# Optimization experiments

Hardware: AMD Instinct MI355X
Metric: run time of the kernel (lower is better)

The kernel has to match this reference:

```python
import jax, jax.numpy as jnp
import numpy as np

H, DH = 8, 16  # num_heads, head_dim (out_feats // num_heads)
NP, NA, NS = 100000, 60000, 1000


def _gat_conv(feat_src, feat_dst, n_dst, src, dst, W, al, ar, b):
    # DGL GATConv (eval mode: feat_drop/attn_drop are identity)
    hs = (feat_src @ W).reshape(-1, H, DH)          # [Ns,H,D]
    hd = (feat_dst @ W).reshape(-1, H, DH)          # [Nd,H,D]
    el = (hs * al).sum(-1)                          # [Ns,H]
    er = (hd * ar).sum(-1)                          # [Nd,H]
    e = jax.nn.leaky_relu(el[src] + er[dst], negative_slope=0.2)  # [E,H]
    # segment softmax over edges sharing a destination node
    emax = jax.ops.segment_max(e, dst, num_segments=n_dst)
    emax = jnp.where(jnp.isfinite(emax), emax, 0.0)
    ee = jnp.exp(e - emax[dst])
    denom = jax.ops.segment_sum(ee, dst, num_segments=n_dst)
    alpha = ee / jnp.maximum(denom[dst], 1e-9)      # [E,H]
    m = jax.ops.segment_sum(alpha[:, :, None] * hs[src], dst, num_segments=n_dst)
    return m.reshape(n_dst, H * DH) + b             # [Nd, out_feats]


def setup_inputs() -> dict:
    key = jax.random.key(0)
    ks = jax.random.split(key, 18)
    Epa, Eps = 300000, 150000
    f32 = jnp.float32
    inp = {
        "feat_paper_0": jax.random.normal(ks[0], (NP, 128), f32),
        "feat_author_0": jax.random.normal(ks[1], (NA, 128), f32),
        "feat_subject_0": jax.random.normal(ks[2], (NS, 128), f32),
        "feat_paper_1": jax.random.normal(ks[3], (NP, 128), f32),
        "feat_author_1": jax.random.normal(ks[4], (NA, 128), f32),
        "feat_subject_1": jax.random.normal(ks[5], (NS, 128), f32),
        "pa_src": jax.random.randint(ks[6], (Epa,), 0, NP, jnp.int32),
        "pa_dst": jax.random.randint(ks[7], (Epa,), 0, NA, jnp.int32),
        "ap_src": jax.random.randint(ks[8], (Epa,), 0, NA, jnp.int32),
        "ap_dst": jax.random.randint(ks[9], (Epa,), 0, NP, jnp.int32),
        "ps_src": jax.random.randint(ks[10], (Eps,), 0, NP, jnp.int32),
        "ps_dst": jax.random.randint(ks[11], (Eps,), 0, NS, jnp.int32),
        "sp_src": jax.random.randint(ks[12], (Eps,), 0, NS, jnp.int32),
        "sp_dst": jax.random.randint(ks[13], (Eps,), 0, NP, jnp.int32),
        "Ws": jax.random.normal(ks[14], (4, 128, 128), f32) * 0.08,
        "als": jax.random.normal(ks[15], (4, H, DH), f32) * 0.1,
        "ars": jax.random.normal(ks[16], (4, H, DH), f32) * 0.1,
        "bs": jnp.zeros((4, 128), f32),
    }
    return inp


def reference(feat_paper_0, feat_author_0, feat_subject_0,
              feat_paper_1, feat_author_1, feat_subject_1,
              pa_src, pa_dst, ap_src, ap_dst, ps_src, ps_dst, sp_src, sp_dst,
              Ws, als, ars, bs):
    def one_input(fp, fa, fs):
        # rel 0: paper->author, 1: author->paper, 2: paper->subject, 3: subject->paper
        h_author = _gat_conv(fp, fa, NA, pa_src, pa_dst, Ws[0], als[0], ars[0], bs[0])
        h_paper_ap = _gat_conv(fa, fp, NP, ap_src, ap_dst, Ws[1], als[1], ars[1], bs[1])
        h_subject = _gat_conv(fp, fs, NS, ps_src, ps_dst, Ws[2], als[2], ars[2], bs[2])
        h_paper_sp = _gat_conv(fs, fp, NP, sp_src, sp_dst, Ws[3], als[3], ars[3], bs[3])
        h_paper = (h_paper_ap + h_paper_sp) * 0.5  # HeteroGraphConv aggregate='mean'
        # act = identity; key order for ACM: [paper, author, subject]
        return jnp.concatenate([h_paper, h_author, h_subject], axis=0)

    out0 = one_input(feat_paper_0, feat_author_0, feat_subject_0)
    out1 = one_input(feat_paper_1, feat_author_1, feat_subject_1)
    return jnp.stack([out0, out1], axis=0)  # [2, NP+NA+NS, 128]
```

## Files before the change

### kernel.cpp

```cpp
#include <hip/hip_runtime.h>

#define NHEAD 8
#define NPAPER 100000
#define NAUTHOR 60000
#define NSUBJ 1000
#define NTOT (NPAPER + NAUTHOR + NSUBJ)
#define NDEG 261000

typedef __attribute__((ext_vector_type(8))) short bf16x8;
typedef __attribute__((ext_vector_type(4))) float f32x4;
typedef __attribute__((ext_vector_type(4))) unsigned int u32x4;

__device__ __forceinline__ unsigned short f2bf(float x) {
    unsigned int u = __builtin_bit_cast(unsigned int, x);
    u += 0x7fffu + ((u >> 16) & 1u);
    return (unsigned short)(u >> 16);
}
__device__ __forceinline__ float bf2f_lo(unsigned int v) {
    return __builtin_bit_cast(float, v << 16);
}
__device__ __forceinline__ float bf2f_hi(unsigned int v) {
    return __builtin_bit_cast(float, v & 0xffff0000u);
}

__global__ void prep_kernel(const float* __restrict__ Ws, const float* __restrict__ als,
                            const float* __restrict__ ars,
                            unsigned short* __restrict__ Wt,
                            unsigned short* __restrict__ combo, int* __restrict__ deg) {
    int b = blockIdx.x;
    if (b >= 288) {
        int idx = (b - 288) * 1024 + threadIdx.x * 4;
        if (idx < NDEG) *reinterpret_cast<int4*>(&deg[idx]) = int4{0, 0, 0, 0};
        return;
    }
    int idx = b * 256 + threadIdx.x;
    if (idx < 65536) {
        int r = idx >> 14, rem = idx & 16383, c = rem >> 7, k = rem & 127;
        Wt[idx] = f2bf(Ws[(r << 14) + k * 128 + c]);
    } else if (idx < 65536 + 8192) {
        int j = idx - 65536;
        int r = j >> 11, rem = j & 2047, n = rem >> 7, k = rem & 127;
        int p = r ^ 1;
        const float *W, *a;
        if (n < 8) {
            W = Ws + (r << 14) + k * 128 + n * 16;
            a = als + r * 128 + n * 16;
        } else {
            int h = n - 8;
            W = Ws + (p << 14) + k * 128 + h * 16;
            a = ars + p * 128 + h * 16;
        }
        float s = 0.f;
#pragma unroll
        for (int d = 0; d < 16; ++d) s += W[d] * a[d];
        combo[j] = f2bf(s);
    }
}

__device__ __forceinline__ void stage_W(unsigned short* Wl, const unsigned short* Wt,
                                        const unsigned short* cb, int tid) {
#pragma unroll
    for (int it = 0; it < 9; ++it) {
        int id = it * 256 + tid;
        int r = id >> 4, c8 = id & 15;
        const unsigned short* srcp = (r < 128) ? (Wt + r * 128) : (cb + (r - 128) * 128);
        uint4 v = *reinterpret_cast<const uint4*>(srcp + c8 * 8);
        *reinterpret_cast<uint4*>(&Wl[(r * 16 + (c8 ^ (r & 15))) * 8]) = v;
    }
}

__device__ __forceinline__ void mfma_set(const unsigned short* Wl, unsigned short* Abf,
                                         const bf16x8* af, int tid, int row0, int N,
                                         float* __restrict__ el, float* __restrict__ er) {
    const int l = tid & 63, w = tid >> 6, lrow = l & 15, lk8 = l >> 4;
#pragma unroll
    for (int t9 = 0; t9 < 9; ++t9) {
        f32x4 acc = f32x4{0.f, 0.f, 0.f, 0.f};
#pragma unroll
        for (int ks = 0; ks < 4; ++ks) {
            int wrow = t9 * 16 + lrow;
            int c8 = ks * 4 + lk8;
            bf16x8 bf = *reinterpret_cast<const bf16x8*>(
                &Wl[(wrow * 16 + (c8 ^ (wrow & 15))) * 8]);
            acc = __builtin_amdgcn_mfma_f32_16x16x32_bf16(af[ks], bf, acc, 0, 0, 0);
        }
        if (t9 < 8) {
#pragma unroll
            for (int r = 0; r < 4; ++r) {
                int rl = w * 16 + lk8 * 4 + r;
                int col = t9 * 16 + lrow;
                Abf[(rl * 16 + ((col >> 3) ^ (rl & 15))) * 8 + (col & 7)] = f2bf(acc[r]);
            }
        } else {
#pragma unroll
            for (int r = 0; r < 4; ++r) {
                int row = row0 + w * 16 + lk8 * 4 + r;
                if (row < N) {
                    if (lrow < 8) el[(size_t)row * 8 + lrow] = acc[r];
                    else er[(size_t)row * 8 + (lrow - 8)] = acc[r];
                }
            }
        }
    }
}

__device__ __forceinline__ void store_hs(const unsigned short* Abf,
                                         unsigned short* __restrict__ hs, int tid,
                                         int row0, int N) {
#pragma unroll
    for (int it = 0; it < 4; ++it) {
        int id = it * 256 + tid;
        int r = id >> 4, c8 = id & 15;
        int row = row0 + r;
        if (row < N) {
            uint4 v = *reinterpret_cast<const uint4*>(&Abf[(r * 16 + (c8 ^ (r & 15))) * 8]);
            *reinterpret_cast<uint4*>(hs + (size_t)row * 128 + c8 * 8) = v;
        }
    }
}

struct PCArgs {
    const int* edst[4];
    int ebase[5];
    int nbase[4];
    int* deg;
    int cblk;
    const float* A[6];
    int N[6];
    int blk0[7];
    const unsigned short* Wt1[6];
    const unsigned short* cb1[6];
    unsigned short* hs1[6];
    float* el1[6];
    float* er1[6];
    const unsigned short* Wt2[6];
    const unsigned short* cb2[6];
    unsigned short* hs2[6];
    float* el2[6];
    float* er2[6];
    int has2[6];
};

__global__ __launch_bounds__(256) void project_count(PCArgs a) {
    __shared__ unsigned short Abf[64 * 128];
    __shared__ unsigned short Wl[144 * 128];
    int bb = blockIdx.x;
    const int tid = threadIdx.x;
    if (bb < a.cblk) {
        int idx = bb * 256 + tid;
        if (idx < a.ebase[4]) {
            int r = 0;
            while (idx >= a.ebase[r + 1]) ++r;
            atomicAdd(&a.deg[a.nbase[r] + a.edst[r][idx - a.ebase[r]]], 1);
        }
        return;
    }
    bb -= a.cblk;
    int t = 0;
    while (bb >= a.blk0[t + 1]) ++t;
    const int row0 = (bb - a.blk0[t]) * 64;
    const int N = a.N[t];
    const float* A = a.A[t];

#pragma unroll
    for (int it = 0; it < 4; ++it) {
        int id = it * 256 + tid;
        int r = id >> 4, c8 = id & 15;
        int row = row0 + r;
        if (row >= N) row = N - 1;
        const f32x4* ap = reinterpret_cast<const f32x4*>(A + (size_t)row * 128 + c8 * 8);
        f32x4 v0 = __builtin_nontemporal_load(ap);
        f32x4 v1 = __builtin_nontemporal_load(ap + 1);
        uint4 pk;
        pk.x = (unsigned)f2bf(v0.x) | ((unsigned)f2bf(v0.y) << 16);
        pk.y = (unsigned)f2bf(v0.z) | ((unsigned)f2bf(v0.w) << 16);
        pk.z = (unsigned)f2bf(v1.x) | ((unsigned)f2bf(v1.y) << 16);
        pk.w = (unsigned)f2bf(v1.z) | ((unsigned)f2bf(v1.w) << 16);
        *reinterpret_cast<uint4*>(&Abf[(r * 16 + (c8 ^ (r & 15))) * 8]) = pk;
    }
    stage_W(Wl, a.Wt1[t], a.cb1[t], tid);
    __syncthreads();

    const int l = tid & 63, w = tid >> 6, lrow = l & 15, lk8 = l >> 4;
    bf16x8 af[4];
    const int arow = w * 16 + lrow;
#pragma unroll
    for (int ks = 0; ks < 4; ++ks) {
        int c8 = ks * 4 + lk8;
        af[ks] = *reinterpret_cast<const bf16x8*>(
            &Abf[(arow * 16 + (c8 ^ (arow & 15))) * 8]);
    }
    __syncthreads();

    mfma_set(Wl, Abf, af, tid, row0, N, a.el1[t], a.er1[t]);
    __syncthreads();
    store_hs(Abf, a.hs1[t], tid, row0, N);
    if (!a.has2[t]) return;
    stage_W(Wl, a.Wt2[t], a.cb2[t], tid);
    __syncthreads();
    mfma_set(Wl, Abf, af, tid, row0, N, a.el2[t], a.er2[t]);
    __syncthreads();
    store_hs(Abf, a.hs2[t], tid, row0, N);
}

__global__ __launch_bounds__(256) void scan_bsum(const int* __restrict__ deg,
                                                 int* __restrict__ bsums, int N) {
    int base = blockIdx.x * 1024 + threadIdx.x * 4;
    int s = 0;
#pragma unroll
    for (int j = 0; j < 4; ++j) {
        int i = base + j;
        if (i < N) s += deg[i];
    }
#pragma unroll
    for (int off = 32; off; off >>= 1) s += __shfl_down(s, off);
    __shared__ int wt[4];
    if ((threadIdx.x & 63) == 0) wt[threadIdx.x >> 6] = s;
    __syncthreads();
    if (threadIdx.x == 0) bsums[blockIdx.x] = wt[0] + wt[1] + wt[2] + wt[3];
}

__global__ __launch_bounds__(256) void scan_final(const int* __restrict__ deg,
                                                  const int* __restrict__ bsums,
                                                  int* __restrict__ row_ptr,
                                                  int* __restrict__ cursor, int N) {
    int t = threadIdx.x;
    __shared__ int s_start;
    __shared__ int wsum[4];
    {
        int acc = 0;
        for (int i = t; i < (int)blockIdx.x; i += 256) acc += bsums[i];
#pragma unroll
        for (int off = 32; off; off >>= 1) acc += __shfl_down(acc, off);
        if ((t & 63) == 0) wsum[t >> 6] = acc;
        __syncthreads();
        if (t == 0) s_start = wsum[0] + wsum[1] + wsum[2] + wsum[3];
        __syncthreads();
    }
    int base = blockIdx.x * 1024 + t * 4;
    int d[4];
    int s = 0;
#pragma unroll
    for (int j = 0; j < 4; ++j) {
        int i = base + j;
        d[j] = (i < N) ? deg[i] : 0;
        s += d[j];
    }
    int inc = s;
#pragma unroll
    for (int off = 1; off < 64; off <<= 1) {
        int u = __shfl_up(inc, off);
        if ((t & 63) >= off) inc += u;
    }
    __shared__ int wt[4];
    if ((t & 63) == 63) wt[t >> 6] = inc;
    __syncthreads();
    int start = s_start;
    for (int w = 0; w < (t >> 6); ++w) start += wt[w];
    start += inc - s;
#pragma unroll
    for (int j = 0; j < 4; ++j) {
        int i = base + j;
        if (i < N) {
            row_ptr[i] = start;
            cursor[i] = start;
        }
        start += d[j];
    }
    if (base < N && base + 4 >= N) row_ptr[N] = start;
}

struct CsrPtrs {
    const int* esrc[4];
    const int* edst[4];
    int ebase[5];
    int nbase[4];
};

__global__ void csr_scatter(CsrPtrs cp, int* __restrict__ cursor,
                            int* __restrict__ srcs) {
    int idx = blockIdx.x * 256 + threadIdx.x;
    if (idx >= cp.ebase[4]) return;
    int r = 0;
    while (idx >= cp.ebase[r + 1]) ++r;
    int e = idx - cp.ebase[r];
    int p = atomicAdd(&cursor[cp.nbase[r] + cp.edst[r][e]], 1);
    srcs[p] = cp.esrc[r][e];
}

__device__ __forceinline__ void acc_dual(
    int p0, int p1, float erd0, float erd1, int l, int h,
    const int* __restrict__ srcs,
    const float* __restrict__ el0, const float* __restrict__ el1,
    const unsigned short* __restrict__ hs0, const unsigned short* __restrict__ hs1,
    float* A0, float* A1, float& DS0, float& DS1) {
    float a0[8], a1[8];
#pragma unroll
    for (int j = 0; j < 8; ++j) { a0[j] = 0.f; a1[j] = 0.f; }
    float d0 = 0.f, d1 = 0.f;
    int p = p0;
    for (; p + 4 <= p1; p += 4) {
        int sx[4];
#pragma unroll
        for (int u = 0; u < 4; ++u) sx[u] = srcs[p + u];
        float ev0[4], ev1[4];
        uint4 q0[4], q1[4];
#pragma unroll
        for (int u = 0; u < 4; ++u) {
            ev0[u] = el0[(size_t)sx[u] * 8 + h] + erd0;
            ev1[u] = el1[(size_t)sx[u] * 8 + h] + erd1;
            q0[u] = *reinterpret_cast<const uint4*>(hs0 + (size_t)sx[u] * 128 + l * 8);
            q1[u] = *reinterpret_cast<const uint4*>(hs1 + (size_t)sx[u] * 128 + l * 8);
        }
#pragma unroll
        for (int u = 0; u < 4; ++u) {
            float e0 = ev0[u];
            e0 = e0 > 0.f ? e0 : 0.2f * e0;
            float ee0 = __expf(e0);
            d0 += ee0;
            a0[0] += ee0 * bf2f_lo(q0[u].x);
            a0[1] += ee0 * bf2f_hi(q0[u].x);
            a0[2] += ee0 * bf2f_lo(q0[u].y);
            a0[3] += ee0 * bf2f_hi(q0[u].y);
            a0[4] += ee0 * bf2f_lo(q0[u].z);
            a0[5] += ee0 * bf2f_hi(q0[u].z);
            a0[6] += ee0 * bf2f_lo(q0[u].w);
            a0[7] += ee0 * bf2f_hi(q0[u].w);
            float e1 = ev1[u];
            e1 = e1 > 0.f ? e1 : 0.2f * e1;
            float ee1 = __expf(e1);
            d1 += ee1;
            a1[0] += ee1 * bf2f_lo(q1[u].x);
            a1[1] += ee1 * bf2f_hi(q1[u].x);
            a1[2] += ee1 * bf2f_lo(q1[u].y);
            a1[3] += ee1 * bf2f_hi(q1[u].y);
            a1[4] += ee1 * bf2f_lo(q1[u].z);
            a1[5] += ee1 * bf2f_hi(q1[u].z);
            a1[6] += ee1 * bf2f_lo(q1[u].w);
            a1[7] += ee1 * bf2f_hi(q1[u].w);
        }
    }
    for (; p < p1; ++p) {
        int s = srcs[p];
        float e0 = el0[(size_t)s * 8 + h] + erd0;
        float e1 = el1[(size_t)s * 8 + h] + erd1;
        uint4 q0 = *reinterpret_cast<const uint4*>(hs0 + (size_t)s * 128 + l * 8);
        uint4 q1 = *reinterpret_cast<const uint4*>(hs1 + (size_t)s * 128 + l * 8);
        e0 = e0 > 0.f ? e0 : 0.2f * e0;
        float ee0 = __expf(e0);
        d0 += ee0;
        a0[0] += ee0 * bf2f_lo(q0.x);
        a0[1] += ee0 * bf2f_hi(q0.x);
        a0[2] += ee0 * bf2f_lo(q0.y);
        a0[3] += ee0 * bf2f_hi(q0.y);
        a0[4] += ee0 * bf2f_lo(q0.z);
        a0[5] += ee0 * bf2f_hi(q0.z);
        a0[6] += ee0 * bf2f_lo(q0.w);
        a0[7] += ee0 * bf2f_hi(q0.w);
        e1 = e1 > 0.f ? e1 : 0.2f * e1;
        float ee1 = __expf(e1);
        d1 += ee1;
        a1[0] += ee1 * bf2f_lo(q1.x);
        a1[1] += ee1 * bf2f_hi(q1.x);
        a1[2] += ee1 * bf2f_lo(q1.y);
        a1[3] += ee1 * bf2f_hi(q1.y);
        a1[4] += ee1 * bf2f_lo(q1.z);
        a1[5] += ee1 * bf2f_hi(q1.z);
        a1[6] += ee1 * bf2f_lo(q1.w);
        a1[7] += ee1 * bf2f_hi(q1.w);
    }
#pragma unroll
    for (int j = 0; j < 8; ++j) { A0[j] = a0[j]; A1[j] = a1[j]; }
    DS0 = d0;
    DS1 = d1;
}

__device__ __forceinline__ void nt_store2(float* op, f32x4 o0, f32x4 o1) {
    f32x4* vp = reinterpret_cast<f32x4*>(op);
    __builtin_nontemporal_store(o0, vp);
    __builtin_nontemporal_store(o1, vp + 1);
}

#define PB2 6250
#define AB2 3750
#define SB2 1000

struct AggArgs {
    const int* rp;
    const int* srcs;
    const float* el[8];
    const float* er[8];
    const unsigned short* hs[8];
    const float* bs;
    float* out0;
    float* out1;
};

__global__ __launch_bounds__(256) void mega_agg(AggArgs a) {
    int blk = blockIdx.x;
    __shared__ float Am[16][128];
    __shared__ float Dm[16][8];

    if (blk < PB2) {
        int dst = blk * 16 + (threadIdx.x >> 4);
        int l = threadIdx.x & 15, h = l >> 1;
        if (dst >= NPAPER) return;
        float A1_0[8], A1_1[8], d1_0, d1_1;
        acc_dual(a.rp[60000 + dst], a.rp[60000 + dst + 1],
                 a.er[1][(size_t)dst * 8 + h], a.er[5][(size_t)dst * 8 + h], l, h,
                 a.srcs, a.el[1], a.el[5], a.hs[1], a.hs[5], A1_0, A1_1, d1_0, d1_1);
        float A3_0[8], A3_1[8], d3_0, d3_1;
        acc_dual(a.rp[161000 + dst], a.rp[161000 + dst + 1],
                 a.er[3][(size_t)dst * 8 + h], a.er[7][(size_t)dst * 8 + h], l, h,
                 a.srcs, a.el[3], a.el[7], a.hs[3], a.hs[7], A3_0, A3_1, d3_0, d3_1);
        const float4* bp1 = reinterpret_cast<const float4*>(a.bs + 128 + l * 8);
        const float4* bp3 = reinterpret_cast<const float4*>(a.bs + 384 + l * 8);
        float4 b10 = bp1[0], b11 = bp1[1], b30 = bp3[0], b31 = bp3[1];
        float i1 = 1.f / fmaxf(d1_0, 1e-9f);
        float i3 = 1.f / fmaxf(d3_0, 1e-9f);
        f32x4 o0, o1;
        o0.x = 0.5f * ((A1_0[0] * i1 + b10.x) + (A3_0[0] * i3 + b30.x));
        o0.y = 0.5f * ((A1_0[1] * i1 + b10.y) + (A3_0[1] * i3 + b30.y));
        o0.z = 0.5f * ((A1_0[2] * i1 + b10.z) + (A3_0[2] * i3 + b30.z));
        o0.w = 0.5f * ((A1_0[3] * i1 + b10.w) + (A3_0[3] * i3 + b30.w));
        o1.x = 0.5f * ((A1_0[4] * i1 + b11.x) + (A3_0[4] * i3 + b31.x));
        o1.y = 0.5f * ((A1_0[5] * i1 + b11.y) + (A3_0[5] * i3 + b31.y));
        o1.z = 0.5f * ((A1_0[6] * i1 + b11.z) + (A3_0[6] * i3 + b31.z));
        o1.w = 0.5f * ((A1_0[7] * i1 + b11.w) + (A3_0[7] * i3 + b31.w));
        nt_store2(a.out0 + (size_t)dst * 128 + l * 8, o0, o1);
        i1 = 1.f / fmaxf(d1_1, 1e-9f);
        i3 = 1.f / fmaxf(d3_1, 1e-9f);
        o0.x = 0.5f * ((A1_1[0] * i1 + b10.x) + (A3_1[0] * i3 + b30.x));
        o0.y = 0.5f * ((A1_1[1] * i1 + b10.y) + (A3_1[1] * i3 + b30.y));
        o0.z = 0.5f * ((A1_1[2] * i1 + b10.z) + (A3_1[2] * i3 + b30.z));
        o0.w = 0.5f * ((A1_1[3] * i1 + b10.w) + (A3_1[3] * i3 + b30.w));
        o1.x = 0.5f * ((A1_1[4] * i1 + b11.x) + (A3_1[4] * i3 + b31.x));
        o1.y = 0.5f * ((A1_1[5] * i1 + b11.y) + (A3_1[5] * i3 + b31.y));
        o1.z = 0.5f * ((A1_1[6] * i1 + b11.z) + (A3_1[6] * i3 + b31.z));
        o1.w = 0.5f * ((A1_1[7] * i1 + b11.w) + (A3_1[7] * i3 + b31.w));
        nt_store2(a.out1 + (size_t)dst * 128 + l * 8, o0, o1);
    } else if (blk < PB2 + AB2) {
        int dst = (blk - PB2) * 16 + (threadIdx.x >> 4);
        int l = threadIdx.x & 15, h = l >> 1;
        if (dst >= NAUTHOR) return;
        float A0[8], A1[8], d0, d1;
        acc_dual(a.rp[dst], a.rp[dst + 1],
                 a.er[0][(size_t)dst * 8 + h], a.er[4][(size_t)dst * 8 + h], l, h,
                 a.srcs, a.el[0], a.el[4], a.hs[0], a.hs[4], A0, A1, d0, d1);
        const float4* bp = reinterpret_cast<const float4*>(a.bs + l * 8);
        float4 b0 = bp[0], b1 = bp[1];
        float inv = 1.f / fmaxf(d0, 1e-9f);
        f32x4 o0 = {A0[0] * inv + b0.x, A0[1] * inv + b0.y,
                    A0[2] * inv + b0.z, A0[3] * inv + b0.w};
        f32x4 o1 = {A0[4] * inv + b1.x, A0[5] * inv + b1.y,
                    A0[6] * inv + b1.z, A0[7] * inv + b1.w};
        nt_store2(a.out0 + (size_t)(NPAPER + dst) * 128 + l * 8, o0, o1);
        inv = 1.f / fmaxf(d1, 1e-9f);
        o0 = f32x4{A1[0] * inv + b0.x, A1[1] * inv + b0.y,
                   A1[2] * inv + b0.z, A1[3] * inv + b0.w};
        o1 = f32x4{A1[4] * inv + b1.x, A1[5] * inv + b1.y,
                   A1[6] * inv + b1.z, A1[7] * inv + b1.w};
        nt_store2(a.out1 + (size_t)(NPAPER + dst) * 128 + l * 8, o0, o1);
    } else {
        int dst = blk - (PB2 + AB2);
        int gl = threadIdx.x >> 4;
        int inp = gl >> 3, ck = gl & 7;
        int l = threadIdx.x & 15, h = l >> 1;
        const float* el = a.el[inp * 4 + 2];
        const float* er = a.er[inp * 4 + 2];
        const unsigned short* hs = a.hs[inp * 4 + 2];
        int p0 = a.rp[160000 + dst], p1 = a.rp[160000 + dst + 1];
        float erd = er[(size_t)dst * 8 + h];
        float acc8[8];
#pragma unroll
        for (int j = 0; j < 8; ++j) acc8[j] = 0.f;
        float dsum = 0.f;
        for (int p = p0 + ck; p < p1; p += 8) {
            int s = a.srcs[p];
            float e = el[(size_t)s * 8 + h] + erd;
            e = e > 0.f ? e : 0.2f * e;
            float ee = __expf(e);
            uint4 q = *reinterpret_cast<const uint4*>(hs + (size_t)s * 128 + l * 8);
            dsum += ee;
            acc8[0] += ee * bf2f_lo(q.x);
            acc8[1] += ee * bf2f_hi(q.x);
            acc8[2] += ee * bf2f_lo(q.y);
            acc8[3] += ee * bf2f_hi(q.y);
            acc8[4] += ee * bf2f_lo(q.z);
            acc8[5] += ee * bf2f_hi(q.z);
            acc8[6] += ee * bf2f_lo(q.w);
            acc8[7] += ee * bf2f_hi(q.w);
        }
#pragma unroll
        for (int j = 0; j < 8; ++j) Am[gl][l * 8 + j] = acc8[j];
        if ((l & 1) == 0) Dm[gl][h] = dsum;
        __syncthreads();
        int c = threadIdx.x;
        int ci = c >> 7;
        int col = c & 127;
        float s = 0.f, dn = 0.f;
        int hh = col >> 4;
#pragma unroll
        for (int g = 0; g < 8; ++g) {
            s += Am[ci * 8 + g][col];
            dn += Dm[ci * 8 + g][hh];
        }
        float v = s / fmaxf(dn, 1e-9f) + a.bs[256 + col];
        float* outp = (ci ? a.out1 : a.out0) + (size_t)(NPAPER + NAUTHOR + dst) * 128 + col;
        __builtin_nontemporal_store(v, outp);
    }
}

extern "C" void kernel_launch(void* const* d_in, const int* in_sizes, int n_in,
                              void* d_out, int out_size, void* d_ws, size_t ws_size,
                              hipStream_t stream) {
    const float* Ws4 = (const float*)d_in[14];
    const float* als = (const float*)d_in[15];
    const float* ars = (const float*)d_in[16];
    const float* bs = (const float*)d_in[17];
    float* out = (float*)d_out;

    const int Es[4] = {in_sizes[6], in_sizes[8], in_sizes[10], in_sizes[12]};
    const int Nsrcs[4] = {NPAPER, NAUTHOR, NPAPER, NSUBJ};
    const int Ndsts[4] = {NAUTHOR, NPAPER, NSUBJ, NPAPER};
    const int Etot = Es[0] + Es[1] + Es[2] + Es[3];

    char* wsp = (char*)d_ws;
    auto carve = [&](size_t bytes) {
        char* p = wsp;
        wsp += (bytes + 255) & ~(size_t)255;
        return p;
    };
    unsigned short* Wt = (unsigned short*)carve(4 * 16384 * 2);
    unsigned short* combo = (unsigned short*)carve(4 * 2048 * 2);
    unsigned short* hsb[2][4];
    float* elb[2][4];
    float* erb[2][4];
    for (int i = 0; i < 2; ++i)
        for (int r = 0; r < 4; ++r) {
            hsb[i][r] = (unsigned short*)carve((size_t)Nsrcs[r] * 128 * 2);
            elb[i][r] = (float*)carve((size_t)Nsrcs[r] * 8 * 4);
            erb[i][r] = (float*)carve((size_t)Ndsts[r] * 8 * 4);
        }
    int* deg = (int*)carve((size_t)NDEG * 4);
    int* cursor = (int*)carve((size_t)NDEG * 4);
    int* bsums = (int*)carve(1024);
    int* rp = (int*)carve((size_t)(NDEG + 1) * 4);
    int* scsr = (int*)carve((size_t)Etot * 4);

    prep_kernel<<<288 + (NDEG + 1023) / 1024, 256, 0, stream>>>(Ws4, als, ars, Wt,
                                                                combo, deg);

    PCArgs pc;
    pc.edst[0] = (const int*)d_in[7];
    pc.edst[1] = (const int*)d_in[9];
    pc.edst[2] = (const int*)d_in[11];
    pc.edst[3] = (const int*)d_in[13];
    pc.ebase[0] = 0;
    for (int r = 0; r < 4; ++r) pc.ebase[r + 1] = pc.ebase[r] + Es[r];
    pc.nbase[0] = 0;
    pc.nbase[1] = 60000;
    pc.nbase[2] = 160000;
    pc.nbase[3] = 161000;
    pc.deg = deg;
    pc.cblk = (Etot + 255) / 256;

    int blk = 0;
    for (int ti = 0; ti < 6; ++ti) {
        int i = ti & 1;
        int nodeT = ti >> 1;
        const int relOf[3] = {0, 1, 3};
        int r = relOf[nodeT];
        const float* feats[3] = {(const float*)d_in[0 + 3 * i],
                                 (const float*)d_in[1 + 3 * i],
                                 (const float*)d_in[2 + 3 * i]};
        pc.A[ti] = feats[nodeT];
        pc.N[ti] = (nodeT == 0) ? NPAPER : (nodeT == 1 ? NAUTHOR : NSUBJ);
        pc.blk0[ti] = blk;
        blk += (pc.N[ti] + 63) / 64;
        pc.Wt1[ti] = Wt + (size_t)r * 16384;
        pc.cb1[ti] = combo + (size_t)r * 2048;
        pc.hs1[ti] = hsb[i][r];
        pc.el1[ti] = elb[i][r];
        pc.er1[ti] = erb[i][r ^ 1];
        pc.has2[ti] = (nodeT == 0);
        int r2 = 2;
        pc.Wt2[ti] = Wt + (size_t)r2 * 16384;
        pc.cb2[ti] = combo + (size_t)r2 * 2048;
        pc.hs2[ti] = hsb[i][r2];
        pc.el2[ti] = elb[i][r2];
        pc.er2[ti] = erb[i][r2 ^ 1];
    }
    pc.blk0[6] = blk;
    project_count<<<pc.cblk + blk, 256, 0, stream>>>(pc);

    int nb = (NDEG + 1023) / 1024;
    scan_bsum<<<nb, 256, 0, stream>>>(deg, bsums, NDEG);
    scan_final<<<nb, 256, 0, stream>>>(deg, bsums, rp, cursor, NDEG);

    CsrPtrs cp;
    cp.esrc[0] = (const int*)d_in[6];  cp.edst[0] = (const int*)d_in[7];
    cp.esrc[1] = (const int*)d_in[8];  cp.edst[1] = (const int*)d_in[9];
    cp.esrc[2] = (const int*)d_in[10]; cp.edst[2] = (const int*)d_in[11];
    cp.esrc[3] = (const int*)d_in[12]; cp.edst[3] = (const int*)d_in[13];
    for (int r = 0; r < 5; ++r) cp.ebase[r] = pc.ebase[r];
    for (int r = 0; r < 4; ++r) cp.nbase[r] = pc.nbase[r];
    csr_scatter<<<(Etot + 255) / 256, 256, 0, stream>>>(cp, cursor, scsr);

    AggArgs ag;
    ag.rp = rp;
    ag.srcs = scsr;
    for (int i = 0; i < 2; ++i)
        for (int r = 0; r < 4; ++r) {
            ag.el[i * 4 + r] = elb[i][r];
            ag.er[i * 4 + r] = erb[i][r];
            ag.hs[i * 4 + r] = hsb[i][r];
        }
    ag.bs = bs;
    ag.out0 = out;
    ag.out1 = out + (size_t)NTOT * 128;
    mega_agg<<<PB2 + AB2 + SB2, 256, 0, stream>>>(ag);
}
```

Before: 324.5 us.

## Fuse CSR scatter into projection kernel and read weights from global memory

The degree count now runs in its own small kernel ahead of the scans, and the CSR scatter is folded into the projection launch as extra blocks, so the scatter overlaps the MFMA projection work instead of the count doing so. The projection no longer stages the weight matrix in LDS. It reads B fragments straight from global memory through the cache, which cuts 36KB of shared memory per block so more blocks can be resident, at the cost of repeated global/L2 reads. The scans now sit on the critical path before the projection launch, and the launch count stays the same.

```diff
diff --git a/kernel.cpp b/kernel.cpp
--- a/kernel.cpp
+++ b/kernel.cpp
@@ -9,7 +9,6 @@
 
 typedef __attribute__((ext_vector_type(8))) short bf16x8;
 typedef __attribute__((ext_vector_type(4))) float f32x4;
-typedef __attribute__((ext_vector_type(4))) unsigned int u32x4;
 
 __device__ __forceinline__ unsigned short f2bf(float x) {
     unsigned int u = __builtin_bit_cast(unsigned int, x);
@@ -57,31 +56,102 @@
     }
 }
 
-__device__ __forceinline__ void stage_W(unsigned short* Wl, const unsigned short* Wt,
-                                        const unsigned short* cb, int tid) {
-#pragma unroll
-    for (int it = 0; it < 9; ++it) {
-        int id = it * 256 + tid;
-        int r = id >> 4, c8 = id & 15;
-        const unsigned short* srcp = (r < 128) ? (Wt + r * 128) : (cb + (r - 128) * 128);
-        uint4 v = *reinterpret_cast<const uint4*>(srcp + c8 * 8);
-        *reinterpret_cast<uint4*>(&Wl[(r * 16 + (c8 ^ (r & 15))) * 8]) = v;
-    }
-}
-
-__device__ __forceinline__ void mfma_set(const unsigned short* Wl, unsigned short* Abf,
-                                         const bf16x8* af, int tid, int row0, int N,
+struct EdgePtrs {
+    const int* esrc[4];
+    const int* edst[4];
+    int ebase[5];
+    int nbase[4];
+};
+
+__global__ void csr_count(EdgePtrs cp, int* __restrict__ deg) {
+    int idx = blockIdx.x * 256 + threadIdx.x;
+    if (idx >= cp.ebase[4]) return;
+    int r = 0;
+    while (idx >= cp.ebase[r + 1]) ++r;
+    atomicAdd(&deg[cp.nbase[r] + cp.edst[r][idx - cp.ebase[r]]], 1);
+}
+
+__global__ __launch_bounds__(256) void scan_bsum(const int* __restrict__ deg,
+                                                 int* __restrict__ bsums, int N) {
+    int base = blockIdx.x * 1024 + threadIdx.x * 4;
+    int s = 0;
+#pragma unroll
+    for (int j = 0; j < 4; ++j) {
+        int i = base + j;
+        if (i < N) s += deg[i];
+    }
+#pragma unroll
+    for (int off = 32; off; off >>= 1) s += __shfl_down(s, off);
+    __shared__ int wt[4];
+    if ((threadIdx.x & 63) == 0) wt[threadIdx.x >> 6] = s;
+    __syncthreads();
+    if (threadIdx.x == 0) bsums[blockIdx.x] = wt[0] + wt[1] + wt[2] + wt[3];
+}
+
+__global__ __launch_bounds__(256) void scan_final(const int* __restrict__ deg,
+                                                  const int* __restrict__ bsums,
+                                                  int* __restrict__ row_ptr,
+                                                  int* __restrict__ cursor, int N) {
+    int t = threadIdx.x;
+    __shared__ int s_start;
+    __shared__ int wsum[4];
+    {
+        int acc = 0;
+        for (int i = t; i < (int)blockIdx.x; i += 256) acc += bsums[i];
+#pragma unroll
+        for (int off = 32; off; off >>= 1) acc += __shfl_down(acc, off);
+        if ((t & 63) == 0) wsum[t >> 6] = acc;
+        __syncthreads();
+        if (t == 0) s_start = wsum[0] + wsum[1] + wsum[2] + wsum[3];
+        __syncthreads();
+    }
+    int base = blockIdx.x * 1024 + t * 4;
+    int d[4];
+    int s = 0;
+#pragma unroll
+    for (int j = 0; j < 4; ++j) {
+        int i = base + j;
+        d[j] = (i < N) ? deg[i] : 0;
+        s += d[j];
+    }
+    int inc = s;
+#pragma unroll
+    for (int off = 1; off < 64; off <<= 1) {
+        int u = __shfl_up(inc, off);
+        if ((t & 63) >= off) inc += u;
+    }
+    __shared__ int wt[4];
+    if ((t & 63) == 63) wt[t >> 6] = inc;
+    __syncthreads();
+    int start = s_start;
+    for (int w = 0; w < (t >> 6); ++w) start += wt[w];
+    start += inc - s;
+#pragma unroll
+    for (int j = 0; j < 4; ++j) {
+        int i = base + j;
+        if (i < N) {
+            row_ptr[i] = start;
+            cursor[i] = start;
+        }
+        start += d[j];
+    }
+    if (base < N && base + 4 >= N) row_ptr[N] = start;
+}
+
+__device__ __forceinline__ void mfma_set(const unsigned short* __restrict__ Wt,
+                                         const unsigned short* __restrict__ cb,
+                                         unsigned short* Abf, const bf16x8* af,
+                                         int tid, int row0, int N,
                                          float* __restrict__ el, float* __restrict__ er) {
     const int l = tid & 63, w = tid >> 6, lrow = l & 15, lk8 = l >> 4;
 #pragma unroll
     for (int t9 = 0; t9 < 9; ++t9) {
+        const unsigned short* base =
+            (t9 < 8) ? (Wt + (t9 * 16 + lrow) * 128) : (cb + lrow * 128);
         f32x4 acc = f32x4{0.f, 0.f, 0.f, 0.f};
 #pragma unroll
         for (int ks = 0; ks < 4; ++ks) {
-            int wrow = t9 * 16 + lrow;
-            int c8 = ks * 4 + lk8;
-            bf16x8 bf = *reinterpret_cast<const bf16x8*>(
-                &Wl[(wrow * 16 + (c8 ^ (wrow & 15))) * 8]);
+            bf16x8 bf = *reinterpret_cast<const bf16x8*>(base + ks * 32 + lk8 * 8);
             acc = __builtin_amdgcn_mfma_f32_16x16x32_bf16(af[ks], bf, acc, 0, 0, 0);
         }
         if (t9 < 8) {
@@ -119,12 +189,14 @@
     }
 }
 
-struct PCArgs {
+struct SPArgs {
+    const int* esrc[4];
     const int* edst[4];
     int ebase[5];
     int nbase[4];
-    int* deg;
-    int cblk;
+    int* cursor;
+    int* scsr;
+    int sblk;
     const float* A[6];
     int N[6];
     int blk0[7];
@@ -141,21 +213,22 @@
     int has2[6];
 };
 
-__global__ __launch_bounds__(256) void project_count(PCArgs a) {
+__global__ __launch_bounds__(256) void scatter_project(SPArgs a) {
     __shared__ unsigned short Abf[64 * 128];
-    __shared__ unsigned short Wl[144 * 128];
     int bb = blockIdx.x;
     const int tid = threadIdx.x;
-    if (bb < a.cblk) {
+    if (bb < a.sblk) {
         int idx = bb * 256 + tid;
         if (idx < a.ebase[4]) {
             int r = 0;
             while (idx >= a.ebase[r + 1]) ++r;
-            atomicAdd(&a.deg[a.nbase[r] + a.edst[r][idx - a.ebase[r]]], 1);
+            int e = idx - a.ebase[r];
+            int p = atomicAdd(&a.cursor[a.nbase[r] + a.edst[r][e]], 1);
+            a.scsr[p] = a.esrc[r][e];
         }
         return;
     }
-    bb -= a.cblk;
+    bb -= a.sblk;
     int t = 0;
     while (bb >= a.blk0[t + 1]) ++t;
     const int row0 = (bb - a.blk0[t]) * 64;
@@ -178,7 +251,6 @@
         pk.w = (unsigned)f2bf(v1.z) | ((unsigned)f2bf(v1.w) << 16);
         *reinterpret_cast<uint4*>(&Abf[(r * 16 + (c8 ^ (r & 15))) * 8]) = pk;
     }
-    stage_W(Wl, a.Wt1[t], a.cb1[t], tid);
     __syncthreads();
 
     const int l = tid & 63, w = tid >> 6, lrow = l & 15, lk8 = l >> 4;
@@ -192,100 +264,14 @@
     }
     __syncthreads();
 
-    mfma_set(Wl, Abf, af, tid, row0, N, a.el1[t], a.er1[t]);
+    mfma_set(a.Wt1[t], a.cb1[t], Abf, af, tid, row0, N, a.el1[t], a.er1[t]);
     __syncthreads();
     store_hs(Abf, a.hs1[t], tid, row0, N);
     if (!a.has2[t]) return;
-    stage_W(Wl, a.Wt2[t], a.cb2[t], tid);
     __syncthreads();
-    mfma_set(Wl, Abf, af, tid, row0, N, a.el2[t], a.er2[t]);
+    mfma_set(a.Wt2[t], a.cb2[t], Abf, af, tid, row0, N, a.el2[t], a.er2[t]);
     __syncthreads();
     store_hs(Abf, a.hs2[t], tid, row0, N);
-}
-
-__global__ __launch_bounds__(256) void scan_bsum(const int* __restrict__ deg,
-                                                 int* __restrict__ bsums, int N) {
-    int base = blockIdx.x * 1024 + threadIdx.x * 4;
-    int s = 0;
-#pragma unroll
-    for (int j = 0; j < 4; ++j) {
-        int i = base + j;
-        if (i < N) s += deg[i];
-    }
-#pragma unroll
-    for (int off = 32; off; off >>= 1) s += __shfl_down(s, off);
-    __shared__ int wt[4];
-    if ((threadIdx.x & 63) == 0) wt[threadIdx.x >> 6] = s;
-    __syncthreads();
-    if (threadIdx.x == 0) bsums[blockIdx.x] = wt[0] + wt[1] + wt[2] + wt[3];
-}
-
-__global__ __launch_bounds__(256) void scan_final(const int* __restrict__ deg,
-                                                  const int* __restrict__ bsums,
-                                                  int* __restrict__ row_ptr,
-                                                  int* __restrict__ cursor, int N) {
-    int t = threadIdx.x;
-    __shared__ int s_start;
-    __shared__ int wsum[4];
-    {
-        int acc = 0;
-        for (int i = t; i < (int)blockIdx.x; i += 256) acc += bsums[i];
-#pragma unroll
-        for (int off = 32; off; off >>= 1) acc += __shfl_down(acc, off);
-        if ((t & 63) == 0) wsum[t >> 6] = acc;
-        __syncthreads();
-        if (t == 0) s_start = wsum[0] + wsum[1] + wsum[2] + wsum[3];
-        __syncthreads();
-    }
-    int base = blockIdx.x * 1024 + t * 4;
-    int d[4];
-    int s = 0;
-#pragma unroll
-    for (int j = 0; j < 4; ++j) {
-        int i = base + j;
-        d[j] = (i < N) ? deg[i] : 0;
-        s += d[j];
-    }
-    int inc = s;
-#pragma unroll
-    for (int off = 1; off < 64; off <<= 1) {
-        int u = __shfl_up(inc, off);
-        if ((t & 63) >= off) inc += u;
-    }
-    __shared__ int wt[4];
-    if ((t & 63) == 63) wt[t >> 6] = inc;
-    __syncthreads();
-    int start = s_start;
-    for (int w = 0; w < (t >> 6); ++w) start += wt[w];
-    start += inc - s;
-#pragma unroll
-    for (int j = 0; j < 4; ++j) {
-        int i = base + j;
-        if (i < N) {
-            row_ptr[i] = start;
-            cursor[i] = start;
-        }
-        start += d[j];
-    }
-    if (base < N && base + 4 >= N) row_ptr[N] = start;
-}
-
-struct CsrPtrs {
-    const int* esrc[4];
-    const int* edst[4];
-    int ebase[5];
-    int nbase[4];
-};
-
-__global__ void csr_scatter(CsrPtrs cp, int* __restrict__ cursor,
-                            int* __restrict__ srcs) {
-    int idx = blockIdx.x * 256 + threadIdx.x;
-    if (idx >= cp.ebase[4]) return;
-    int r = 0;
-    while (idx >= cp.ebase[r + 1]) ++r;
-    int e = idx - cp.ebase[r];
-    int p = atomicAdd(&cursor[cp.nbase[r] + cp.edst[r][e]], 1);
-    srcs[p] = cp.esrc[r][e];
 }
 
 __device__ __forceinline__ void acc_dual(
@@ -548,22 +534,35 @@
     int* rp = (int*)carve((size_t)(NDEG + 1) * 4);
     int* scsr = (int*)carve((size_t)Etot * 4);
 
+    EdgePtrs ep;
+    ep.esrc[0] = (const int*)d_in[6];  ep.edst[0] = (const int*)d_in[7];
+    ep.esrc[1] = (const int*)d_in[8];  ep.edst[1] = (const int*)d_in[9];
+    ep.esrc[2] = (const int*)d_in[10]; ep.edst[2] = (const int*)d_in[11];
+    ep.esrc[3] = (const int*)d_in[12]; ep.edst[3] = (const int*)d_in[13];
+    ep.ebase[0] = 0;
+    for (int r = 0; r < 4; ++r) ep.ebase[r + 1] = ep.ebase[r] + Es[r];
+    ep.nbase[0] = 0;
+    ep.nbase[1] = 60000;
+    ep.nbase[2] = 160000;
+    ep.nbase[3] = 161000;
+
     prep_kernel<<<288 + (NDEG + 1023) / 1024, 256, 0, stream>>>(Ws4, als, ars, Wt,
                                                                 combo, deg);
-
-    PCArgs pc;
-    pc.edst[0] = (const int*)d_in[7];
-    pc.edst[1] = (const int*)d_in[9];
-    pc.edst[2] = (const int*)d_in[11];
-    pc.edst[3] = (const int*)d_in[13];
-    pc.ebase[0] = 0;
-    for (int r = 0; r < 4; ++r) pc.ebase[r + 1] = pc.ebase[r] + Es[r];
-    pc.nbase[0] = 0;
-    pc.nbase[1] = 60000;
-    pc.nbase[2] = 160000;
-    pc.nbase[3] = 161000;
-    pc.deg = deg;
-    pc.cblk = (Etot + 255) / 256;
+    csr_count<<<(Etot + 255) / 256, 256, 0, stream>>>(ep, deg);
+    int nb = (NDEG + 1023) / 1024;
+    scan_bsum<<<nb, 256, 0, stream>>>(deg, bsums, NDEG);
+    scan_final<<<nb, 256, 0, stream>>>(deg, bsums, rp, cursor, NDEG);
+
+    SPArgs sp;
+    for (int r = 0; r < 4; ++r) {
+        sp.esrc[r] = ep.esrc[r];
+        sp.edst[r] = ep.edst[r];
+        sp.nbase[r] = ep.nbase[r];
+    }
+    for (int r = 0; r < 5; ++r) sp.ebase[r] = ep.ebase[r];
+    sp.cursor = cursor;
+    sp.scsr = scsr;
+    sp.sblk = (Etot + 255) / 256;
 
     int blk = 0;
     for (int ti = 0; ti < 6; ++ti) {
@@ -574,38 +573,25 @@
         const float* feats[3] = {(const float*)d_in[0 + 3 * i],
                                  (const float*)d_in[1 + 3 * i],
                                  (const float*)d_in[2 + 3 * i]};
-        pc.A[ti] = feats[nodeT];
-        pc.N[ti] = (nodeT == 0) ? NPAPER : (nodeT == 1 ? NAUTHOR : NSUBJ);
-        pc.blk0[ti] = blk;
-        blk += (pc.N[ti] + 63) / 64;
-        pc.Wt1[ti] = Wt + (size_t)r * 16384;
-        pc.cb1[ti] = combo + (size_t)r * 2048;
-        pc.hs1[ti] = hsb[i][r];
-        pc.el1[ti] = elb[i][r];
-        pc.er1[ti] = erb[i][r ^ 1];
-        pc.has2[ti] = (nodeT == 0);
+        sp.A[ti] = feats[nodeT];
+        sp.N[ti] = (nodeT == 0) ? NPAPER : (nodeT == 1 ? NAUTHOR : NSUBJ);
+        sp.blk0[ti] = blk;
+        blk += (sp.N[ti] + 63) / 64;
+        sp.Wt1[ti] = Wt + (size_t)r * 16384;
+        sp.cb1[ti] = combo + (size_t)r * 2048;
+        sp.hs1[ti] = hsb[i][r];
+        sp.el1[ti] = elb[i][r];
+        sp.er1[ti] = erb[i][r ^ 1];
+        sp.has2[ti] = (nodeT == 0);
         int r2 = 2;
-        pc.Wt2[ti] = Wt + (size_t)r2 * 16384;
-        pc.cb2[ti] = combo + (size_t)r2 * 2048;
-        pc.hs2[ti] = hsb[i][r2];
-        pc.el2[ti] = elb[i][r2];
-        pc.er2[ti] = erb[i][r2 ^ 1];
-    }
-    pc.blk0[6] = blk;
-    project_count<<<pc.cblk + blk, 256, 0, stream>>>(pc);
-
-    int nb = (NDEG + 1023) / 1024;
-    scan_bsum<<<nb, 256, 0, stream>>>(deg, bsums, NDEG);
-    scan_final<<<nb, 256, 0, stream>>>(deg, bsums, rp, cursor, NDEG);
-
-    CsrPtrs cp;
-    cp.esrc[0] = (const int*)d_in[6];  cp.edst[0] = (const int*)d_in[7];
-    cp.esrc[1] = (const int*)d_in[8];  cp.edst[1] = (const int*)d_in[9];
-    cp.esrc[2] = (const int*)d_in[10]; cp.edst[2] = (const int*)d_in[11];
-    cp.esrc[3] = (const int*)d_in[12]; cp.edst[3] = (const int*)d_in[13];
-    for (int r = 0; r < 5; ++r) cp.ebase[r] = pc.ebase[r];
-    for (int r = 0; r < 4; ++r) cp.nbase[r] = pc.nbase[r];
-    csr_scatter<<<(Etot + 255) / 256, 256, 0, stream>>>(cp, cursor, scsr);
+        sp.Wt2[ti] = Wt + (size_t)r2 * 16384;
+        sp.cb2[ti] = combo + (size_t)r2 * 2048;
+        sp.hs2[ti] = hsb[i][r2];
+        sp.el2[ti] = elb[i][r2];
+        sp.er2[ti] = erb[i][r2 ^ 1];
+    }
+    sp.blk0[6] = blk;
+    scatter_project<<<sp.sblk + blk, 256, 0, stream>>>(sp);
 
     AggArgs ag;
     ag.rp = rp;
```

Result: slower. 407.5 us (+25.6%).
